# Performance work log

Hardware: AMD Instinct MI355X
Metric: run time of the kernel (lower is better)

Reference implementation:

```python
import jax, jax.numpy as jnp
import numpy as np

N = 100000       # nodes
F_IN = 512       # input features
H = 16           # hidden dim of conv1
C = 5            # num classes
E = 6400000      # edges (avg degree 64)


def setup_inputs() -> dict:
    key = jax.random.key(0)
    ks = jax.random.split(key, 8)
    x = jax.random.normal(ks[0], (N, F_IN), dtype=jnp.float32)
    edge_index = jax.random.randint(ks[1], (2, E), 0, N, dtype=jnp.int64)
    W1 = jax.random.normal(ks[2], (F_IN, H), dtype=jnp.float32) * (1.0 / np.sqrt(F_IN))
    b1 = jnp.zeros((H,), jnp.float32)
    W2 = jax.random.normal(ks[3], (H, C), dtype=jnp.float32) * (1.0 / np.sqrt(H))
    b2 = jnp.zeros((C,), jnp.float32)
    W3 = jax.random.normal(ks[4], (C, 32), dtype=jnp.float32) * (1.0 / np.sqrt(C))
    b3 = jnp.zeros((32,), jnp.float32)
    W4 = jax.random.normal(ks[5], (32, C), dtype=jnp.float32) * (1.0 / np.sqrt(32))
    b4 = jnp.zeros((C,), jnp.float32)
    return {"x": x, "edge_index": edge_index, "W1": W1, "b1": b1,
            "W2": W2, "b2": b2, "W3": W3, "b3": b3, "W4": W4, "b4": b4}


def _gcn_norm(edge_index):
    # add self-loops, unit edge weights (data has no edge_attr)
    loop = jnp.arange(N, dtype=edge_index.dtype)
    src = jnp.concatenate([edge_index[0], loop])
    dst = jnp.concatenate([edge_index[1], loop])
    deg = jax.ops.segment_sum(jnp.ones_like(dst, dtype=jnp.float32), dst,
                              num_segments=N)
    dinv = jnp.where(deg > 0, jax.lax.rsqrt(jnp.maximum(deg, 1.0)), 0.0)
    norm = dinv[src] * dinv[dst]  # [E+N]
    return src, dst, norm


def _gcn_conv(x, src, dst, norm, W, b):
    h = x @ W                               # transform first (small out dim)
    msg = h[src] * norm[:, None]            # gather + edge-normalize
    out = jax.ops.segment_sum(msg, dst, num_segments=N)  # scatter-add
    return out + b


def reference(x, edge_index, W1, b1, W2, b2, W3, b3, W4, b4):
    src, dst, norm = _gcn_norm(edge_index)
    h = _gcn_conv(x, src, dst, norm, W1, b1)
    h = jax.nn.relu(h)
    # F.dropout(training=self.training): identity in eval mode
    h = _gcn_conv(h, src, dst, norm, W2, b2)
    h = jax.nn.relu(h @ W3 + b3)
    h = h @ W4 + b4
    return jax.nn.log_softmax(h, axis=1)
```

## Files before the change

kernel.cpp:

```cpp
#include <hip/hip_runtime.h>
#include <hip/hip_bf16.h>


#define F_IN 512
#define HDIM 16
#define CDIM 5
#define NB   1024
#define SEG  8192
#define GWP_STRIDE 16
#define EPT  10
#define SCHUNK (1024*EPT)
#define CAP  8192

typedef __attribute__((ext_vector_type(8))) short short8;
typedef __attribute__((ext_vector_type(4))) float floatx4;

__device__ inline float bf2f(unsigned short u){
  unsigned int i = ((unsigned int)u) << 16; float f; __builtin_memcpy(&f, &i, 4); return f;
}
__device__ inline unsigned short f2bf(float x){
  unsigned int i; __builtin_memcpy(&i, &x, 4);
  unsigned int r = i + 0x7FFFu + ((i >> 16) & 1u);
  return (unsigned short)(r >> 16);
}
__device__ inline float ulo(unsigned int u){
  unsigned int v = u << 16; float f; __builtin_memcpy(&f, &v, 4); return f;
}
__device__ inline float uhi(unsigned int u){
  unsigned int v = u & 0xFFFF0000u; float f; __builtin_memcpy(&f, &v, 4); return f;
}
__device__ inline short8 pack8(float4 u0, float4 u1){
  unsigned short o[8] = {f2bf(u0.x), f2bf(u0.y), f2bf(u0.z), f2bf(u0.w),
                         f2bf(u1.x), f2bf(u1.y), f2bf(u1.z), f2bf(u1.w)};
  short8 r; __builtin_memcpy(&r, o, 16); return r;
}

__global__ __launch_bounds__(1024) void k_detect(const int* __restrict__ ei, int* __restrict__ flag,
                                                 int* __restrict__ gwp, int E){
  int t = threadIdx.x;
  if (t == 0) *flag = 0;
  gwp[t * GWP_STRIDE] = t * SEG;
  __syncthreads();
  long long step = E / 1024; if (step < 1) step = 1;
  long long pos = 2LL * ((long long)t * step) + 1;
  if (pos < 2LL * E){
    if (ei[pos] != 0) atomicOr(flag, 1);
  }
}

__global__ __launch_bounds__(256) void k_packW1(const float* __restrict__ W1,
                                                unsigned short* __restrict__ pw){
  int s = threadIdx.x;
  for (int slot = s; slot < 1024; slot += 256){
    int col = slot & 15, kg = (slot >> 4) & 3, t = slot >> 6;
    unsigned short o[8];
    #pragma unroll
    for (int e = 0; e < 8; ++e)
      o[e] = f2bf(W1[(t * 32 + kg * 8 + e) * HDIM + col]);
    uint4 v; __builtin_memcpy(&v, o, 16);
    *(uint4*)(pw + (size_t)slot * 8) = v;
  }
}

__global__ __launch_bounds__(1024) void k_binscatter(const int* __restrict__ ei, const int* __restrict__ flag,
                                                     int* __restrict__ gwp, int* __restrict__ pairs,
                                                     int E, int NPB){
  __shared__ int bh[NB];
  __shared__ int lex[NB + 1];
  __shared__ int bb2[NB];
  __shared__ int wsum[16];
  __shared__ unsigned short kb[SCHUNK];
  __shared__ int stage[SCHUNK];
  int t = threadIdx.x;
  int e0 = blockIdx.x * SCHUNK;
  int e1 = min(E, e0 + SCHUNK);
  int cnt = e1 - e0;
  if (cnt <= 0) return;
  int is32 = *flag;
  const uint2* ei2 = (const uint2*)ei;
  int pk[EPT]; int bi[EPT];
  #pragma unroll
  for (int j = 0; j < EPT; ++j){
    int e = e0 + t + j * 1024;
    if (e < e1){
      int src, dst;
      if (is32){ src = ei[e]; dst = ei[(size_t)E + e]; }
      else     { src = (int)ei2[e].x; dst = (int)ei2[(size_t)E + e].x; }
      int b = dst / NPB;
      pk[j] = src | ((dst - b * NPB) << 20);
      bi[j] = b;
    } else bi[j] = -1;
  }
  bh[t] = 0;
  __syncthreads();
  #pragma unroll
  for (int j = 0; j < EPT; ++j) if (bi[j] >= 0) atomicAdd(&bh[bi[j]], 1);
  __syncthreads();
  {
    int lane = t & 63, w = t >> 6;
    int v = bh[t];
    int xs = v;
    #pragma unroll
    for (int off = 1; off < 64; off <<= 1){
      int y = __shfl_up(xs, off);
      if (lane >= off) xs += y;
    }
    if (lane == 63) wsum[w] = xs;
    __syncthreads();
    int woff = 0;
    for (int k = 0; k < w; ++k) woff += wsum[k];
    int excl = woff + xs - v;
    lex[t] = excl;
    if (t == 1023) lex[NB] = woff + xs;
    bb2[t] = v ? atomicAdd(&gwp[t * GWP_STRIDE], v) : 0;
    __syncthreads();
    bh[t] = excl;
  }
  __syncthreads();
  #pragma unroll
  for (int j = 0; j < EPT; ++j){
    if (bi[j] >= 0){
      int idx = atomicAdd(&bh[bi[j]], 1);
      stage[idx] = pk[j];
      kb[idx] = (unsigned short)bi[j];
    }
  }
  __syncthreads();
  for (int k = t; k < cnt; k += 1024){
    int b = kb[k];
    pairs[bb2[b] + (k - lex[b])] = stage[k];
  }
}

__global__ __launch_bounds__(1024) void k_scanNB(const int* __restrict__ gwp, int* __restrict__ bbase,
                                                 int nb){
  __shared__ int wsum[16];
  int t = threadIdx.x, lane = t & 63, w = t >> 6;
  int v = (t < nb) ? (gwp[t * GWP_STRIDE] - t * SEG) : 0;
  int xs = v;
  #pragma unroll
  for (int off = 1; off < 64; off <<= 1){
    int y = __shfl_up(xs, off);
    if (lane >= off) xs += y;
  }
  if (lane == 63) wsum[w] = xs;
  __syncthreads();
  int woff = 0;
  for (int k = 0; k < w; ++k) woff += wsum[k];
  if (t < nb) bbase[t] = woff + xs - v;
  if (t == 1023) bbase[nb] = woff + xs;
}

__global__ __launch_bounds__(512) void k_bucket(const int* __restrict__ pairs, const int* __restrict__ bbase,
                                                int* __restrict__ rowptr, float* __restrict__ dinv,
                                                int* __restrict__ ssrc, int NPB, int n, int Etot){
  __shared__ int lcnt[4][128];
  __shared__ int tot[128];
  __shared__ int lexcl[128];
  __shared__ int w0sum;
  __shared__ int stage[CAP];
  int b = blockIdx.x;
  int t = threadIdx.x;
  int g = t >> 7;
  int node0 = b * NPB;
  int pbase = b * SEG;
  int obase = bbase[b];
  int cntE = bbase[b + 1] - obase;
  lcnt[g][t & 127] = 0;
  __syncthreads();
  for (int k = t; k < cntE; k += 512){
    unsigned int v = (unsigned int)pairs[pbase + k];
    atomicAdd(&lcnt[g][v >> 20], 1);
  }
  __syncthreads();
  if (t < 128){
    int s0 = lcnt[0][t], s1 = lcnt[1][t], s2 = lcnt[2][t], s3 = lcnt[3][t];
    tot[t] = s0 + s1 + s2 + s3;
    lcnt[0][t] = 0; lcnt[1][t] = s0; lcnt[2][t] = s0 + s1; lcnt[3][t] = s0 + s1 + s2;
  }
  __syncthreads();
  int lane = t & 63;
  int v = (t < 128) ? tot[t] : 0;
  int xs = v;
  #pragma unroll
  for (int off = 1; off < 64; off <<= 1){
    int y = __shfl_up(xs, off);
    if (lane >= off) xs += y;
  }
  if (t == 63) w0sum = xs;
  __syncthreads();
  if (t < 128) lexcl[t] = xs - v + ((t >= 64) ? w0sum : 0);
  __syncthreads();
  if (t < NPB){
    int node = node0 + t;
    if (node < n){
      rowptr[node] = obase + lexcl[t];
      dinv[node] = rsqrtf((float)(tot[t] + 1));
    }
  }
  lcnt[g][t & 127] += lexcl[t & 127];
  if (b == 0 && t == 0) rowptr[n] = Etot;
  __syncthreads();
  for (int k = t; k < cntE; k += 512){
    unsigned int v2 = (unsigned int)pairs[pbase + k];
    int idx = atomicAdd(&lcnt[g][v2 >> 20], 1);
    int src = (int)(v2 & 0xFFFFFu);
    if (idx < CAP) stage[idx] = src;
    else ssrc[obase + idx] = src;
  }
  __syncthreads();
  int m = cntE < CAP ? cntE : CAP;
  for (int k = t; k < m; k += 512) ssrc[obase + k] = stage[k];
}

__global__ __launch_bounds__(256) void k_gemm1(const float* __restrict__ x, const unsigned short* __restrict__ pw,
                                               const float* __restrict__ dinv, unsigned short* __restrict__ hs1,
                                               int n){
  int lane = threadIdx.x & 63;
  int col = lane & 15;
  int kg  = lane >> 4;
  int nt = (n + 15) >> 4;
  const short8* pw8 = (const short8*)pw;
  short8 B[16];
  #pragma unroll
  for (int t = 0; t < 16; ++t) B[t] = pw8[t * 64 + kg * 16 + col];
  int nw = gridDim.x * 4;
  for (int wid = blockIdx.x * 4 + (threadIdx.x >> 6); wid < nt; wid += nw){
    int row = wid * 16 + col;
    const float* xr = x + (size_t)min(row, n - 1) * F_IN;
    floatx4 acc = {0.f, 0.f, 0.f, 0.f};
    #pragma unroll
    for (int t = 0; t < 16; ++t){
      const float4* p = (const float4*)(xr + t * 32 + kg * 8);
      float4 u0 = p[0];
      float4 u1 = p[1];
      acc = __builtin_amdgcn_mfma_f32_16x16x32_bf16(pack8(u0, u1), B[t], acc, 0, 0, 0);
    }
    #pragma unroll
    for (int r = 0; r < 4; ++r){
      int orow = wid * 16 + kg * 4 + r;
      if (orow < n) hs1[(size_t)orow * HDIM + col] = f2bf(dinv[orow] * acc[r]);
    }
  }
}

__global__ __launch_bounds__(256) void k_agg1(const unsigned short* __restrict__ hs1,
    const int* __restrict__ rowptr, const int* __restrict__ ssrc,
    const float* __restrict__ dinv, const float* __restrict__ b1,
    const float* __restrict__ W2, unsigned short* __restrict__ hs2, int n){
  int lane = threadIdx.x & 63;
  int i = blockIdx.x * 4 + (threadIdx.x >> 6);
  if (i >= n) return;
  int slot = lane >> 1, half = lane & 1;
  int beg = rowptr[i], end = rowptr[i + 1];
  const uint4* hv = (const uint4*)hs1;
  float acc[8];
  #pragma unroll
  for (int k = 0; k < 8; ++k) acc[k] = 0.f;
  for (int e = beg + slot; e < end; e += 32){
    int src = ssrc[e];
    uint4 v = hv[(size_t)src * 2 + half];
    acc[0] += ulo(v.x); acc[1] += uhi(v.x);
    acc[2] += ulo(v.y); acc[3] += uhi(v.y);
    acc[4] += ulo(v.z); acc[5] += uhi(v.z);
    acc[6] += ulo(v.w); acc[7] += uhi(v.w);
  }
  #pragma unroll
  for (int off = 2; off < 64; off <<= 1){
    #pragma unroll
    for (int k = 0; k < 8; ++k) acc[k] += __shfl_xor(acc[k], off);
  }
  uint4 sv = hv[(size_t)i * 2 + half];
  float self[8] = {ulo(sv.x), uhi(sv.x), ulo(sv.y), uhi(sv.y),
                   ulo(sv.z), uhi(sv.z), ulo(sv.w), uhi(sv.w)};
  float dv = dinv[i];
  const float4* b1v = (const float4*)b1;
  float4 bl = b1v[half * 2], bh = b1v[half * 2 + 1];
  float r[8];
  r[0] = fmaxf(fmaf(dv, acc[0] + self[0], bl.x), 0.f);
  r[1] = fmaxf(fmaf(dv, acc[1] + self[1], bl.y), 0.f);
  r[2] = fmaxf(fmaf(dv, acc[2] + self[2], bl.z), 0.f);
  r[3] = fmaxf(fmaf(dv, acc[3] + self[3], bl.w), 0.f);
  r[4] = fmaxf(fmaf(dv, acc[4] + self[4], bh.x), 0.f);
  r[5] = fmaxf(fmaf(dv, acc[5] + self[5], bh.y), 0.f);
  r[6] = fmaxf(fmaf(dv, acc[6] + self[6], bh.z), 0.f);
  r[7] = fmaxf(fmaf(dv, acc[7] + self[7], bh.w), 0.f);
  const float* w2 = W2 + half * 8 * CDIM;
  float p[CDIM];
  #pragma unroll
  for (int c = 0; c < CDIM; ++c){
    float s = 0.f;
    #pragma unroll
    for (int k = 0; k < 8; ++k) s = fmaf(r[k], w2[k * CDIM + c], s);
    p[c] = s;
  }
  #pragma unroll
  for (int c = 0; c < CDIM; ++c) p[c] += __shfl_xor(p[c], 1);
  if (lane == 0){
    unsigned short o[8];
    #pragma unroll
    for (int c = 0; c < CDIM; ++c) o[c] = f2bf(dv * p[c]);
    o[5] = 0; o[6] = 0; o[7] = 0;
    uint4 v; __builtin_memcpy(&v, o, 16);
    *(uint4*)(hs2 + (size_t)i * 8) = v;
  }
}

__global__ __launch_bounds__(256) void k_agg2(const unsigned short* __restrict__ hs2,
    const int* __restrict__ rowptr, const int* __restrict__ ssrc,
    const float* __restrict__ dinv, const float* __restrict__ b2,
    const float* __restrict__ W3, const float* __restrict__ b3,
    const float* __restrict__ W4, const float* __restrict__ b4,
    float* __restrict__ out, int n){
  int lane = threadIdx.x & 63;
  int i = blockIdx.x * 4 + (threadIdx.x >> 6);
  if (i >= n) return;
  int beg = rowptr[i], end = rowptr[i + 1];
  const uint4* hv = (const uint4*)hs2;
  float acc[CDIM];
  #pragma unroll
  for (int k = 0; k < CDIM; ++k) acc[k] = 0.f;
  for (int e = beg + lane; e < end; e += 64){
    int src = ssrc[e];
    uint4 v = hv[src];
    acc[0] += ulo(v.x); acc[1] += uhi(v.x);
    acc[2] += ulo(v.y); acc[3] += uhi(v.y);
    acc[4] += ulo(v.z);
  }
  #pragma unroll
  for (int off = 1; off < 64; off <<= 1){
    #pragma unroll
    for (int k = 0; k < CDIM; ++k) acc[k] += __shfl_xor(acc[k], off);
  }
  float dv = dinv[i];
  uint4 sv = hv[i];
  float a0 = fmaf(dv, acc[0] + ulo(sv.x), b2[0]);
  float a1 = fmaf(dv, acc[1] + uhi(sv.x), b2[1]);
  float a2 = fmaf(dv, acc[2] + ulo(sv.y), b2[2]);
  float a3 = fmaf(dv, acc[3] + uhi(sv.y), b2[3]);
  float a4 = fmaf(dv, acc[4] + ulo(sv.z), b2[4]);
  int m = lane & 31;
  float h3 = b3[m];
  h3 = fmaf(a0, W3[0 * 32 + m], h3);
  h3 = fmaf(a1, W3[1 * 32 + m], h3);
  h3 = fmaf(a2, W3[2 * 32 + m], h3);
  h3 = fmaf(a3, W3[3 * 32 + m], h3);
  h3 = fmaf(a4, W3[4 * 32 + m], h3);
  h3 = fmaxf(h3, 0.f);
  float q0 = h3 * W4[m * CDIM + 0], q1 = h3 * W4[m * CDIM + 1], q2 = h3 * W4[m * CDIM + 2];
  float q3 = h3 * W4[m * CDIM + 3], q4 = h3 * W4[m * CDIM + 4];
  #pragma unroll
  for (int off = 1; off < 32; off <<= 1){
    q0 += __shfl_xor(q0, off); q1 += __shfl_xor(q1, off); q2 += __shfl_xor(q2, off);
    q3 += __shfl_xor(q3, off); q4 += __shfl_xor(q4, off);
  }
  q0 += b4[0]; q1 += b4[1]; q2 += b4[2]; q3 += b4[3]; q4 += b4[4];
  float mx = fmaxf(fmaxf(fmaxf(q0, q1), fmaxf(q2, q3)), q4);
  float sum = expf(q0 - mx) + expf(q1 - mx) + expf(q2 - mx) + expf(q3 - mx) + expf(q4 - mx);
  float lse = mx + logf(sum);
  if (lane < CDIM){
    float v = q0;
    if (lane == 1) v = q1;
    if (lane == 2) v = q2;
    if (lane == 3) v = q3;
    if (lane == 4) v = q4;
    out[(size_t)i * CDIM + lane] = v - lse;
  }
}

extern "C" void kernel_launch(void* const* d_in, const int* in_sizes, int n_in,
                              void* d_out, int out_size, void* d_ws, size_t ws_size,
                              hipStream_t stream){
  const float* x  = (const float*)d_in[0];
  const int*   ei = (const int*)d_in[1];
  const float* W1 = (const float*)d_in[2];
  const float* b1 = (const float*)d_in[3];
  const float* W2 = (const float*)d_in[4];
  const float* b2 = (const float*)d_in[5];
  const float* W3 = (const float*)d_in[6];
  const float* b3 = (const float*)d_in[7];
  const float* W4 = (const float*)d_in[8];
  const float* b4 = (const float*)d_in[9];
  float* out = (float*)d_out;

  int N = in_sizes[0] / F_IN;
  int E = in_sizes[1] / 2;
  int NPB = (N + NB - 1) / NB;

  char* ws = (char*)d_ws;
  size_t off = 0;
  auto alloc = [&](size_t bytes) -> char* {
    char* p = ws + off;
    off += (bytes + 255) & ~(size_t)255;
    return p;
  };
  int* flag  = (int*)alloc(4);
  int* gwp   = (int*)alloc((size_t)NB * GWP_STRIDE * 4);
  int* bbase = (int*)alloc(((size_t)NB + 1) * 4);
  int* rowptr= (int*)alloc(((size_t)N + 1) * 4);
  float* dinv= (float*)alloc((size_t)N * 4);
  unsigned short* pw = (unsigned short*)alloc((size_t)F_IN * HDIM * 2);
  int* pairs = (int*)alloc((size_t)NB * SEG * 4);
  int* ssrc  = (int*)alloc((size_t)E * 4);
  unsigned short* hs1 = (unsigned short*)alloc((size_t)N * HDIM * 2);
  unsigned short* hs2 = (unsigned short*)alloc((size_t)N * 8 * 2);
  (void)ws_size; (void)n_in; (void)out_size;

  k_detect<<<1, 1024, 0, stream>>>(ei, flag, gwp, E);
  k_packW1<<<1, 256, 0, stream>>>(W1, pw);
  int sblocks = (E + SCHUNK - 1) / SCHUNK;
  k_binscatter<<<sblocks, 1024, 0, stream>>>(ei, flag, gwp, pairs, E, NPB);
  k_scanNB<<<1, 1024, 0, stream>>>(gwp, bbase, NB);
  k_bucket<<<NB, 512, 0, stream>>>(pairs, bbase, rowptr, dinv, ssrc, NPB, N, E);
  k_gemm1<<<768, 256, 0, stream>>>(x, pw, dinv, hs1, N);
  k_agg1<<<(N + 3) / 4, 256, 0, stream>>>(hs1, rowptr, ssrc, dinv, b1, W2, hs2, N);
  k_agg2<<<(N + 3) / 4, 256, 0, stream>>>(hs2, rowptr, ssrc, dinv, b2, W3, b3, W4, b4, out, N);
}
```

Before: 265.4 us.

## Drop CSR build; aggregate directly from destination buckets with shared-memory atomics

Removes the scan and per-node bucket sort that built rowptr and sorted sources. Aggregation now reads the coarse destination-binned pairs per bucket (512 buckets of about 196 nodes) and accumulates messages into LDS with float atomics. A small kernel computes degrees from the same bins. This saves a full pass that rewrites 6.4M edges, at the cost of heavy LDS atomic contention and fewer, larger blocks. The final per-node MLP is also moved into a single thread per node.

```diff
diff --git a/kernel.cpp b/kernel.cpp
--- a/kernel.cpp
+++ b/kernel.cpp
@@ -5,12 +5,12 @@
 #define F_IN 512
 #define HDIM 16
 #define CDIM 5
-#define NB   1024
-#define SEG  8192
+#define NB   512
+#define NPB_MAX 200
+#define SEG  16384
 #define GWP_STRIDE 16
 #define EPT  10
 #define SCHUNK (1024*EPT)
-#define CAP  8192
 
 typedef __attribute__((ext_vector_type(8))) short short8;
 typedef __attribute__((ext_vector_type(4))) float floatx4;
@@ -39,7 +39,7 @@
                                                  int* __restrict__ gwp, int E){
   int t = threadIdx.x;
   if (t == 0) *flag = 0;
-  gwp[t * GWP_STRIDE] = t * SEG;
+  if (t < NB) gwp[t * GWP_STRIDE] = t * SEG;
   __syncthreads();
   long long step = E / 1024; if (step < 1) step = 1;
   long long pos = 2LL * ((long long)t * step) + 1;
@@ -91,14 +91,14 @@
       bi[j] = b;
     } else bi[j] = -1;
   }
-  bh[t] = 0;
+  if (t < NB) bh[t] = 0;
   __syncthreads();
   #pragma unroll
   for (int j = 0; j < EPT; ++j) if (bi[j] >= 0) atomicAdd(&bh[bi[j]], 1);
   __syncthreads();
   {
     int lane = t & 63, w = t >> 6;
-    int v = bh[t];
+    int v = (t < NB) ? bh[t] : 0;
     int xs = v;
     #pragma unroll
     for (int off = 1; off < 64; off <<= 1){
@@ -110,11 +110,12 @@
     int woff = 0;
     for (int k = 0; k < w; ++k) woff += wsum[k];
     int excl = woff + xs - v;
-    lex[t] = excl;
-    if (t == 1023) lex[NB] = woff + xs;
-    bb2[t] = v ? atomicAdd(&gwp[t * GWP_STRIDE], v) : 0;
-    __syncthreads();
-    bh[t] = excl;
+    if (t < NB){
+      lex[t] = excl;
+      bb2[t] = v ? atomicAdd(&gwp[t * GWP_STRIDE], v) : 0;
+      bh[t] = excl;
+    }
+    if (t == NB - 1) lex[NB] = excl + v;
   }
   __syncthreads();
   #pragma unroll
@@ -132,85 +133,20 @@
   }
 }
 
-__global__ __launch_bounds__(1024) void k_scanNB(const int* __restrict__ gwp, int* __restrict__ bbase,
-                                                 int nb){
-  __shared__ int wsum[16];
-  int t = threadIdx.x, lane = t & 63, w = t >> 6;
-  int v = (t < nb) ? (gwp[t * GWP_STRIDE] - t * SEG) : 0;
-  int xs = v;
-  #pragma unroll
-  for (int off = 1; off < 64; off <<= 1){
-    int y = __shfl_up(xs, off);
-    if (lane >= off) xs += y;
-  }
-  if (lane == 63) wsum[w] = xs;
-  __syncthreads();
-  int woff = 0;
-  for (int k = 0; k < w; ++k) woff += wsum[k];
-  if (t < nb) bbase[t] = woff + xs - v;
-  if (t == 1023) bbase[nb] = woff + xs;
-}
-
-__global__ __launch_bounds__(512) void k_bucket(const int* __restrict__ pairs, const int* __restrict__ bbase,
-                                                int* __restrict__ rowptr, float* __restrict__ dinv,
-                                                int* __restrict__ ssrc, int NPB, int n, int Etot){
-  __shared__ int lcnt[4][128];
-  __shared__ int tot[128];
-  __shared__ int lexcl[128];
-  __shared__ int w0sum;
-  __shared__ int stage[CAP];
-  int b = blockIdx.x;
-  int t = threadIdx.x;
-  int g = t >> 7;
-  int node0 = b * NPB;
-  int pbase = b * SEG;
-  int obase = bbase[b];
-  int cntE = bbase[b + 1] - obase;
-  lcnt[g][t & 127] = 0;
-  __syncthreads();
-  for (int k = t; k < cntE; k += 512){
-    unsigned int v = (unsigned int)pairs[pbase + k];
-    atomicAdd(&lcnt[g][v >> 20], 1);
-  }
-  __syncthreads();
-  if (t < 128){
-    int s0 = lcnt[0][t], s1 = lcnt[1][t], s2 = lcnt[2][t], s3 = lcnt[3][t];
-    tot[t] = s0 + s1 + s2 + s3;
-    lcnt[0][t] = 0; lcnt[1][t] = s0; lcnt[2][t] = s0 + s1; lcnt[3][t] = s0 + s1 + s2;
-  }
-  __syncthreads();
-  int lane = t & 63;
-  int v = (t < 128) ? tot[t] : 0;
-  int xs = v;
-  #pragma unroll
-  for (int off = 1; off < 64; off <<= 1){
-    int y = __shfl_up(xs, off);
-    if (lane >= off) xs += y;
-  }
-  if (t == 63) w0sum = xs;
-  __syncthreads();
-  if (t < 128) lexcl[t] = xs - v + ((t >= 64) ? w0sum : 0);
-  __syncthreads();
-  if (t < NPB){
-    int node = node0 + t;
-    if (node < n){
-      rowptr[node] = obase + lexcl[t];
-      dinv[node] = rsqrtf((float)(tot[t] + 1));
-    }
-  }
-  lcnt[g][t & 127] += lexcl[t & 127];
-  if (b == 0 && t == 0) rowptr[n] = Etot;
-  __syncthreads();
-  for (int k = t; k < cntE; k += 512){
-    unsigned int v2 = (unsigned int)pairs[pbase + k];
-    int idx = atomicAdd(&lcnt[g][v2 >> 20], 1);
-    int src = (int)(v2 & 0xFFFFFu);
-    if (idx < CAP) stage[idx] = src;
-    else ssrc[obase + idx] = src;
-  }
-  __syncthreads();
-  int m = cntE < CAP ? cntE : CAP;
-  for (int k = t; k < m; k += 512) ssrc[obase + k] = stage[k];
+__global__ __launch_bounds__(256) void k_deg(const int* __restrict__ pairs, const int* __restrict__ gwp,
+                                             float* __restrict__ dinv, int n, int NPB){
+  __shared__ int h[NPB_MAX];
+  int b = blockIdx.x, t = threadIdx.x;
+  int cntE = gwp[b * GWP_STRIDE] - b * SEG;
+  for (int k = t; k < NPB; k += 256) h[k] = 0;
+  __syncthreads();
+  const int* pb = pairs + (size_t)b * SEG;
+  for (int k = t; k < cntE; k += 256) atomicAdd(&h[((unsigned)pb[k]) >> 20], 1);
+  __syncthreads();
+  for (int k = t; k < NPB; k += 256){
+    int node = b * NPB + k;
+    if (node < n) dinv[node] = rsqrtf((float)(h[k] + 1));
+  }
 }
 
 __global__ __launch_bounds__(256) void k_gemm1(const float* __restrict__ x, const unsigned short* __restrict__ pw,
@@ -244,127 +180,113 @@
   }
 }
 
-__global__ __launch_bounds__(256) void k_agg1(const unsigned short* __restrict__ hs1,
-    const int* __restrict__ rowptr, const int* __restrict__ ssrc,
+__global__ __launch_bounds__(512) void k_agg1f(const unsigned short* __restrict__ hs1,
+    const int* __restrict__ pairs, const int* __restrict__ gwp,
     const float* __restrict__ dinv, const float* __restrict__ b1,
-    const float* __restrict__ W2, unsigned short* __restrict__ hs2, int n){
-  int lane = threadIdx.x & 63;
-  int i = blockIdx.x * 4 + (threadIdx.x >> 6);
-  if (i >= n) return;
-  int slot = lane >> 1, half = lane & 1;
-  int beg = rowptr[i], end = rowptr[i + 1];
+    const float* __restrict__ W2, unsigned short* __restrict__ hs2, int n, int NPB){
+  __shared__ float acc[NPB_MAX * 17];
+  int b = blockIdx.x, t = threadIdx.x;
+  int cntE = gwp[b * GWP_STRIDE] - b * SEG;
+  for (int k = t; k < NPB * 17; k += 512) acc[k] = 0.f;
+  __syncthreads();
   const uint4* hv = (const uint4*)hs1;
-  float acc[8];
-  #pragma unroll
-  for (int k = 0; k < 8; ++k) acc[k] = 0.f;
-  for (int e = beg + slot; e < end; e += 32){
-    int src = ssrc[e];
+  const int* pb = pairs + (size_t)b * SEG;
+  int half = t & 1;
+  for (int k = (t >> 1); k < cntE; k += 256){
+    int p = pb[k];
+    int src = p & 0xFFFFF;
+    int dl = ((unsigned)p) >> 20;
     uint4 v = hv[(size_t)src * 2 + half];
-    acc[0] += ulo(v.x); acc[1] += uhi(v.x);
-    acc[2] += ulo(v.y); acc[3] += uhi(v.y);
-    acc[4] += ulo(v.z); acc[5] += uhi(v.z);
-    acc[6] += ulo(v.w); acc[7] += uhi(v.w);
-  }
-  #pragma unroll
-  for (int off = 2; off < 64; off <<= 1){
-    #pragma unroll
-    for (int k = 0; k < 8; ++k) acc[k] += __shfl_xor(acc[k], off);
-  }
-  uint4 sv = hv[(size_t)i * 2 + half];
-  float self[8] = {ulo(sv.x), uhi(sv.x), ulo(sv.y), uhi(sv.y),
-                   ulo(sv.z), uhi(sv.z), ulo(sv.w), uhi(sv.w)};
-  float dv = dinv[i];
-  const float4* b1v = (const float4*)b1;
-  float4 bl = b1v[half * 2], bh = b1v[half * 2 + 1];
-  float r[8];
-  r[0] = fmaxf(fmaf(dv, acc[0] + self[0], bl.x), 0.f);
-  r[1] = fmaxf(fmaf(dv, acc[1] + self[1], bl.y), 0.f);
-  r[2] = fmaxf(fmaf(dv, acc[2] + self[2], bl.z), 0.f);
-  r[3] = fmaxf(fmaf(dv, acc[3] + self[3], bl.w), 0.f);
-  r[4] = fmaxf(fmaf(dv, acc[4] + self[4], bh.x), 0.f);
-  r[5] = fmaxf(fmaf(dv, acc[5] + self[5], bh.y), 0.f);
-  r[6] = fmaxf(fmaf(dv, acc[6] + self[6], bh.z), 0.f);
-  r[7] = fmaxf(fmaf(dv, acc[7] + self[7], bh.w), 0.f);
-  const float* w2 = W2 + half * 8 * CDIM;
-  float p[CDIM];
-  #pragma unroll
-  for (int c = 0; c < CDIM; ++c){
-    float s = 0.f;
-    #pragma unroll
-    for (int k = 0; k < 8; ++k) s = fmaf(r[k], w2[k * CDIM + c], s);
-    p[c] = s;
-  }
-  #pragma unroll
-  for (int c = 0; c < CDIM; ++c) p[c] += __shfl_xor(p[c], 1);
-  if (lane == 0){
+    float* a = acc + dl * 17 + half * 8;
+    atomicAdd(a + 0, ulo(v.x)); atomicAdd(a + 1, uhi(v.x));
+    atomicAdd(a + 2, ulo(v.y)); atomicAdd(a + 3, uhi(v.y));
+    atomicAdd(a + 4, ulo(v.z)); atomicAdd(a + 5, uhi(v.z));
+    atomicAdd(a + 6, ulo(v.w)); atomicAdd(a + 7, uhi(v.w));
+  }
+  __syncthreads();
+  for (int i = t; i < NPB; i += 512){
+    int node = b * NPB + i;
+    if (node >= n) break;
+    float dv = dinv[node];
+    uint4 s0 = hv[(size_t)node * 2], s1 = hv[(size_t)node * 2 + 1];
+    float self[16] = {ulo(s0.x), uhi(s0.x), ulo(s0.y), uhi(s0.y),
+                      ulo(s0.z), uhi(s0.z), ulo(s0.w), uhi(s0.w),
+                      ulo(s1.x), uhi(s1.x), ulo(s1.y), uhi(s1.y),
+                      ulo(s1.z), uhi(s1.z), ulo(s1.w), uhi(s1.w)};
+    float r[16];
+    #pragma unroll
+    for (int j = 0; j < 16; ++j)
+      r[j] = fmaxf(fmaf(dv, acc[i * 17 + j] + self[j], b1[j]), 0.f);
     unsigned short o[8];
     #pragma unroll
-    for (int c = 0; c < CDIM; ++c) o[c] = f2bf(dv * p[c]);
+    for (int c = 0; c < CDIM; ++c){
+      float s = 0.f;
+      #pragma unroll
+      for (int j = 0; j < 16; ++j) s = fmaf(r[j], W2[j * CDIM + c], s);
+      o[c] = f2bf(dv * s);
+    }
     o[5] = 0; o[6] = 0; o[7] = 0;
     uint4 v; __builtin_memcpy(&v, o, 16);
-    *(uint4*)(hs2 + (size_t)i * 8) = v;
-  }
-}
-
-__global__ __launch_bounds__(256) void k_agg2(const unsigned short* __restrict__ hs2,
-    const int* __restrict__ rowptr, const int* __restrict__ ssrc,
+    *(uint4*)(hs2 + (size_t)node * 8) = v;
+  }
+}
+
+__global__ __launch_bounds__(512) void k_agg2f(const unsigned short* __restrict__ hs2,
+    const int* __restrict__ pairs, const int* __restrict__ gwp,
     const float* __restrict__ dinv, const float* __restrict__ b2,
     const float* __restrict__ W3, const float* __restrict__ b3,
     const float* __restrict__ W4, const float* __restrict__ b4,
-    float* __restrict__ out, int n){
-  int lane = threadIdx.x & 63;
-  int i = blockIdx.x * 4 + (threadIdx.x >> 6);
-  if (i >= n) return;
-  int beg = rowptr[i], end = rowptr[i + 1];
+    float* __restrict__ out, int n, int NPB){
+  __shared__ float acc[NPB_MAX * 9];
+  int b = blockIdx.x, t = threadIdx.x;
+  int cntE = gwp[b * GWP_STRIDE] - b * SEG;
+  for (int k = t; k < NPB * 9; k += 512) acc[k] = 0.f;
+  __syncthreads();
   const uint4* hv = (const uint4*)hs2;
-  float acc[CDIM];
-  #pragma unroll
-  for (int k = 0; k < CDIM; ++k) acc[k] = 0.f;
-  for (int e = beg + lane; e < end; e += 64){
-    int src = ssrc[e];
+  const int* pb = pairs + (size_t)b * SEG;
+  for (int k = t; k < cntE; k += 512){
+    int p = pb[k];
+    int src = p & 0xFFFFF;
+    int dl = ((unsigned)p) >> 20;
     uint4 v = hv[src];
-    acc[0] += ulo(v.x); acc[1] += uhi(v.x);
-    acc[2] += ulo(v.y); acc[3] += uhi(v.y);
-    acc[4] += ulo(v.z);
-  }
-  #pragma unroll
-  for (int off = 1; off < 64; off <<= 1){
-    #pragma unroll
-    for (int k = 0; k < CDIM; ++k) acc[k] += __shfl_xor(acc[k], off);
-  }
-  float dv = dinv[i];
-  uint4 sv = hv[i];
-  float a0 = fmaf(dv, acc[0] + ulo(sv.x), b2[0]);
-  float a1 = fmaf(dv, acc[1] + uhi(sv.x), b2[1]);
-  float a2 = fmaf(dv, acc[2] + ulo(sv.y), b2[2]);
-  float a3 = fmaf(dv, acc[3] + uhi(sv.y), b2[3]);
-  float a4 = fmaf(dv, acc[4] + ulo(sv.z), b2[4]);
-  int m = lane & 31;
-  float h3 = b3[m];
-  h3 = fmaf(a0, W3[0 * 32 + m], h3);
-  h3 = fmaf(a1, W3[1 * 32 + m], h3);
-  h3 = fmaf(a2, W3[2 * 32 + m], h3);
-  h3 = fmaf(a3, W3[3 * 32 + m], h3);
-  h3 = fmaf(a4, W3[4 * 32 + m], h3);
-  h3 = fmaxf(h3, 0.f);
-  float q0 = h3 * W4[m * CDIM + 0], q1 = h3 * W4[m * CDIM + 1], q2 = h3 * W4[m * CDIM + 2];
-  float q3 = h3 * W4[m * CDIM + 3], q4 = h3 * W4[m * CDIM + 4];
-  #pragma unroll
-  for (int off = 1; off < 32; off <<= 1){
-    q0 += __shfl_xor(q0, off); q1 += __shfl_xor(q1, off); q2 += __shfl_xor(q2, off);
-    q3 += __shfl_xor(q3, off); q4 += __shfl_xor(q4, off);
-  }
-  q0 += b4[0]; q1 += b4[1]; q2 += b4[2]; q3 += b4[3]; q4 += b4[4];
-  float mx = fmaxf(fmaxf(fmaxf(q0, q1), fmaxf(q2, q3)), q4);
-  float sum = expf(q0 - mx) + expf(q1 - mx) + expf(q2 - mx) + expf(q3 - mx) + expf(q4 - mx);
-  float lse = mx + logf(sum);
-  if (lane < CDIM){
-    float v = q0;
-    if (lane == 1) v = q1;
-    if (lane == 2) v = q2;
-    if (lane == 3) v = q3;
-    if (lane == 4) v = q4;
-    out[(size_t)i * CDIM + lane] = v - lse;
+    float* a = acc + dl * 9;
+    atomicAdd(a + 0, ulo(v.x)); atomicAdd(a + 1, uhi(v.x));
+    atomicAdd(a + 2, ulo(v.y)); atomicAdd(a + 3, uhi(v.y));
+    atomicAdd(a + 4, ulo(v.z));
+  }
+  __syncthreads();
+  for (int i = t; i < NPB; i += 512){
+    int node = b * NPB + i;
+    if (node >= n) break;
+    float dv = dinv[node];
+    uint4 sv = hv[node];
+    float a0 = fmaf(dv, acc[i * 9 + 0] + ulo(sv.x), b2[0]);
+    float a1 = fmaf(dv, acc[i * 9 + 1] + uhi(sv.x), b2[1]);
+    float a2 = fmaf(dv, acc[i * 9 + 2] + ulo(sv.y), b2[2]);
+    float a3 = fmaf(dv, acc[i * 9 + 3] + uhi(sv.y), b2[3]);
+    float a4 = fmaf(dv, acc[i * 9 + 4] + ulo(sv.z), b2[4]);
+    float q[CDIM];
+    #pragma unroll
+    for (int c = 0; c < CDIM; ++c) q[c] = b4[c];
+    #pragma unroll
+    for (int m = 0; m < 32; ++m){
+      float h3 = b3[m];
+      h3 = fmaf(a0, W3[0 * 32 + m], h3);
+      h3 = fmaf(a1, W3[1 * 32 + m], h3);
+      h3 = fmaf(a2, W3[2 * 32 + m], h3);
+      h3 = fmaf(a3, W3[3 * 32 + m], h3);
+      h3 = fmaf(a4, W3[4 * 32 + m], h3);
+      h3 = fmaxf(h3, 0.f);
+      #pragma unroll
+      for (int c = 0; c < CDIM; ++c) q[c] = fmaf(h3, W4[m * CDIM + c], q[c]);
+    }
+    float mx = fmaxf(fmaxf(fmaxf(q[0], q[1]), fmaxf(q[2], q[3])), q[4]);
+    float sum = expf(q[0] - mx) + expf(q[1] - mx) + expf(q[2] - mx) +
+                expf(q[3] - mx) + expf(q[4] - mx);
+    float lse = mx + logf(sum);
+    float* op = out + (size_t)node * CDIM;
+    #pragma unroll
+    for (int c = 0; c < CDIM; ++c) op[c] = q[c] - lse;
   }
 }
 
@@ -396,12 +318,9 @@
   };
   int* flag  = (int*)alloc(4);
   int* gwp   = (int*)alloc((size_t)NB * GWP_STRIDE * 4);
-  int* bbase = (int*)alloc(((size_t)NB + 1) * 4);
-  int* rowptr= (int*)alloc(((size_t)N + 1) * 4);
   float* dinv= (float*)alloc((size_t)N * 4);
   unsigned short* pw = (unsigned short*)alloc((size_t)F_IN * HDIM * 2);
   int* pairs = (int*)alloc((size_t)NB * SEG * 4);
-  int* ssrc  = (int*)alloc((size_t)E * 4);
   unsigned short* hs1 = (unsigned short*)alloc((size_t)N * HDIM * 2);
   unsigned short* hs2 = (unsigned short*)alloc((size_t)N * 8 * 2);
   (void)ws_size; (void)n_in; (void)out_size;
@@ -410,9 +329,8 @@
   k_packW1<<<1, 256, 0, stream>>>(W1, pw);
   int sblocks = (E + SCHUNK - 1) / SCHUNK;
   k_binscatter<<<sblocks, 1024, 0, stream>>>(ei, flag, gwp, pairs, E, NPB);
-  k_scanNB<<<1, 1024, 0, stream>>>(gwp, bbase, NB);
-  k_bucket<<<NB, 512, 0, stream>>>(pairs, bbase, rowptr, dinv, ssrc, NPB, N, E);
+  k_deg<<<NB, 256, 0, stream>>>(pairs, gwp, dinv, N, NPB);
   k_gemm1<<<768, 256, 0, stream>>>(x, pw, dinv, hs1, N);
-  k_agg1<<<(N + 3) / 4, 256, 0, stream>>>(hs1, rowptr, ssrc, dinv, b1, W2, hs2, N);
-  k_agg2<<<(N + 3) / 4, 256, 0, stream>>>(hs2, rowptr, ssrc, dinv, b2, W3, b3, W4, b4, out, N);
-}
+  k_agg1f<<<NB, 512, 0, stream>>>(hs1, pairs, gwp, dinv, b1, W2, hs2, N, NPB);
+  k_agg2f<<<NB, 512, 0, stream>>>(hs2, pairs, gwp, dinv, b2, W3, b3, W4, b4, out, N, NPB);
+}
```

After: 802.2 us. 3.02x slower.

## Drop global bucket scan and pack kernel; use padded per-bucket CSR with row degrees

Applied to the files above, without the earlier changes.

Removes the k_scanNB and k_packW1 launches. W1 packing is folded into k_detect, and the CSR is laid out with a fixed SEG-sized segment per bucket, so each row is described by a start offset plus a stored degree instead of a globally compacted row pointer. k_bucket now uses 8 per-wave histogram copies instead of 4, which should reduce LDS atomic contention. The cost is a larger ssrc buffer and an extra rowdeg read in the aggregation kernels, and gather locality may drop slightly because segments are padded.

```diff
diff --git a/kernel.cpp b/kernel.cpp
--- a/kernel.cpp
+++ b/kernel.cpp
@@ -36,10 +36,20 @@
 }
 
 __global__ __launch_bounds__(1024) void k_detect(const int* __restrict__ ei, int* __restrict__ flag,
-                                                 int* __restrict__ gwp, int E){
+                                                 int* __restrict__ gwp, const float* __restrict__ W1,
+                                                 unsigned short* __restrict__ pw, int E){
   int t = threadIdx.x;
   if (t == 0) *flag = 0;
   gwp[t * GWP_STRIDE] = t * SEG;
+  {
+    int col = t & 15, kg = (t >> 4) & 3, tt = t >> 6;
+    unsigned short o[8];
+    #pragma unroll
+    for (int e = 0; e < 8; ++e)
+      o[e] = f2bf(W1[(tt * 32 + kg * 8 + e) * HDIM + col]);
+    uint4 v; __builtin_memcpy(&v, o, 16);
+    *(uint4*)(pw + (size_t)t * 8) = v;
+  }
   __syncthreads();
   long long step = E / 1024; if (step < 1) step = 1;
   long long pos = 2LL * ((long long)t * step) + 1;
@@ -48,25 +58,11 @@
   }
 }
 
-__global__ __launch_bounds__(256) void k_packW1(const float* __restrict__ W1,
-                                                unsigned short* __restrict__ pw){
-  int s = threadIdx.x;
-  for (int slot = s; slot < 1024; slot += 256){
-    int col = slot & 15, kg = (slot >> 4) & 3, t = slot >> 6;
-    unsigned short o[8];
-    #pragma unroll
-    for (int e = 0; e < 8; ++e)
-      o[e] = f2bf(W1[(t * 32 + kg * 8 + e) * HDIM + col]);
-    uint4 v; __builtin_memcpy(&v, o, 16);
-    *(uint4*)(pw + (size_t)slot * 8) = v;
-  }
-}
-
 __global__ __launch_bounds__(1024) void k_binscatter(const int* __restrict__ ei, const int* __restrict__ flag,
                                                      int* __restrict__ gwp, int* __restrict__ pairs,
                                                      int E, int NPB){
   __shared__ int bh[NB];
-  __shared__ int lex[NB + 1];
+  __shared__ int lex[NB];
   __shared__ int bb2[NB];
   __shared__ int wsum[16];
   __shared__ unsigned short kb[SCHUNK];
@@ -111,7 +107,6 @@
     for (int k = 0; k < w; ++k) woff += wsum[k];
     int excl = woff + xs - v;
     lex[t] = excl;
-    if (t == 1023) lex[NB] = woff + xs;
     bb2[t] = v ? atomicAdd(&gwp[t * GWP_STRIDE], v) : 0;
     __syncthreads();
     bh[t] = excl;
@@ -132,41 +127,23 @@
   }
 }
 
-__global__ __launch_bounds__(1024) void k_scanNB(const int* __restrict__ gwp, int* __restrict__ bbase,
-                                                 int nb){
-  __shared__ int wsum[16];
-  int t = threadIdx.x, lane = t & 63, w = t >> 6;
-  int v = (t < nb) ? (gwp[t * GWP_STRIDE] - t * SEG) : 0;
-  int xs = v;
-  #pragma unroll
-  for (int off = 1; off < 64; off <<= 1){
-    int y = __shfl_up(xs, off);
-    if (lane >= off) xs += y;
-  }
-  if (lane == 63) wsum[w] = xs;
-  __syncthreads();
-  int woff = 0;
-  for (int k = 0; k < w; ++k) woff += wsum[k];
-  if (t < nb) bbase[t] = woff + xs - v;
-  if (t == 1023) bbase[nb] = woff + xs;
-}
-
-__global__ __launch_bounds__(512) void k_bucket(const int* __restrict__ pairs, const int* __restrict__ bbase,
-                                                int* __restrict__ rowptr, float* __restrict__ dinv,
-                                                int* __restrict__ ssrc, int NPB, int n, int Etot){
-  __shared__ int lcnt[4][128];
+__global__ __launch_bounds__(512) void k_bucket(const int* __restrict__ pairs, const int* __restrict__ gwp,
+                                                int* __restrict__ rowptr, int* __restrict__ rowdeg,
+                                                float* __restrict__ dinv, int* __restrict__ ssrc,
+                                                int NPB, int n){
+  __shared__ int lcnt[8][128];
   __shared__ int tot[128];
   __shared__ int lexcl[128];
   __shared__ int w0sum;
   __shared__ int stage[CAP];
   int b = blockIdx.x;
   int t = threadIdx.x;
-  int g = t >> 7;
+  int g = t >> 6;
   int node0 = b * NPB;
   int pbase = b * SEG;
-  int obase = bbase[b];
-  int cntE = bbase[b + 1] - obase;
-  lcnt[g][t & 127] = 0;
+  int obase = b * SEG;
+  int cntE = gwp[b * GWP_STRIDE] - b * SEG;
+  for (int k = t & 63; k < 128; k += 64) lcnt[g][k] = 0;
   __syncthreads();
   for (int k = t; k < cntE; k += 512){
     unsigned int v = (unsigned int)pairs[pbase + k];
@@ -174,9 +151,14 @@
   }
   __syncthreads();
   if (t < 128){
-    int s0 = lcnt[0][t], s1 = lcnt[1][t], s2 = lcnt[2][t], s3 = lcnt[3][t];
-    tot[t] = s0 + s1 + s2 + s3;
-    lcnt[0][t] = 0; lcnt[1][t] = s0; lcnt[2][t] = s0 + s1; lcnt[3][t] = s0 + s1 + s2;
+    int c = 0;
+    #pragma unroll
+    for (int gg = 0; gg < 8; ++gg){
+      int tmp = lcnt[gg][t];
+      lcnt[gg][t] = c;
+      c += tmp;
+    }
+    tot[t] = c;
   }
   __syncthreads();
   int lane = t & 63;
@@ -195,11 +177,14 @@
     int node = node0 + t;
     if (node < n){
       rowptr[node] = obase + lexcl[t];
+      rowdeg[node] = tot[t];
       dinv[node] = rsqrtf((float)(tot[t] + 1));
     }
   }
-  lcnt[g][t & 127] += lexcl[t & 127];
-  if (b == 0 && t == 0) rowptr[n] = Etot;
+  if (t < 128){
+    #pragma unroll
+    for (int gg = 0; gg < 8; ++gg) lcnt[gg][t] += lexcl[t];
+  }
   __syncthreads();
   for (int k = t; k < cntE; k += 512){
     unsigned int v2 = (unsigned int)pairs[pbase + k];
@@ -245,14 +230,14 @@
 }
 
 __global__ __launch_bounds__(256) void k_agg1(const unsigned short* __restrict__ hs1,
-    const int* __restrict__ rowptr, const int* __restrict__ ssrc,
+    const int* __restrict__ rowptr, const int* __restrict__ rowdeg, const int* __restrict__ ssrc,
     const float* __restrict__ dinv, const float* __restrict__ b1,
     const float* __restrict__ W2, unsigned short* __restrict__ hs2, int n){
   int lane = threadIdx.x & 63;
   int i = blockIdx.x * 4 + (threadIdx.x >> 6);
   if (i >= n) return;
   int slot = lane >> 1, half = lane & 1;
-  int beg = rowptr[i], end = rowptr[i + 1];
+  int beg = rowptr[i], end = beg + rowdeg[i];
   const uint4* hv = (const uint4*)hs1;
   float acc[8];
   #pragma unroll
@@ -307,7 +292,7 @@
 }
 
 __global__ __launch_bounds__(256) void k_agg2(const unsigned short* __restrict__ hs2,
-    const int* __restrict__ rowptr, const int* __restrict__ ssrc,
+    const int* __restrict__ rowptr, const int* __restrict__ rowdeg, const int* __restrict__ ssrc,
     const float* __restrict__ dinv, const float* __restrict__ b2,
     const float* __restrict__ W3, const float* __restrict__ b3,
     const float* __restrict__ W4, const float* __restrict__ b4,
@@ -315,7 +300,7 @@
   int lane = threadIdx.x & 63;
   int i = blockIdx.x * 4 + (threadIdx.x >> 6);
   if (i >= n) return;
-  int beg = rowptr[i], end = rowptr[i + 1];
+  int beg = rowptr[i], end = beg + rowdeg[i];
   const uint4* hv = (const uint4*)hs2;
   float acc[CDIM];
   #pragma unroll
@@ -396,23 +381,21 @@
   };
   int* flag  = (int*)alloc(4);
   int* gwp   = (int*)alloc((size_t)NB * GWP_STRIDE * 4);
-  int* bbase = (int*)alloc(((size_t)NB + 1) * 4);
-  int* rowptr= (int*)alloc(((size_t)N + 1) * 4);
+  int* rowptr= (int*)alloc((size_t)N * 4);
+  int* rowdeg= (int*)alloc((size_t)N * 4);
   float* dinv= (float*)alloc((size_t)N * 4);
   unsigned short* pw = (unsigned short*)alloc((size_t)F_IN * HDIM * 2);
   int* pairs = (int*)alloc((size_t)NB * SEG * 4);
-  int* ssrc  = (int*)alloc((size_t)E * 4);
+  int* ssrc  = (int*)alloc((size_t)NB * SEG * 4);
   unsigned short* hs1 = (unsigned short*)alloc((size_t)N * HDIM * 2);
   unsigned short* hs2 = (unsigned short*)alloc((size_t)N * 8 * 2);
   (void)ws_size; (void)n_in; (void)out_size;
 
-  k_detect<<<1, 1024, 0, stream>>>(ei, flag, gwp, E);
-  k_packW1<<<1, 256, 0, stream>>>(W1, pw);
+  k_detect<<<1, 1024, 0, stream>>>(ei, flag, gwp, W1, pw, E);
   int sblocks = (E + SCHUNK - 1) / SCHUNK;
   k_binscatter<<<sblocks, 1024, 0, stream>>>(ei, flag, gwp, pairs, E, NPB);
-  k_scanNB<<<1, 1024, 0, stream>>>(gwp, bbase, NB);
-  k_bucket<<<NB, 512, 0, stream>>>(pairs, bbase, rowptr, dinv, ssrc, NPB, N, E);
+  k_bucket<<<NB, 512, 0, stream>>>(pairs, gwp, rowptr, rowdeg, dinv, ssrc, NPB, N);
   k_gemm1<<<768, 256, 0, stream>>>(x, pw, dinv, hs1, N);
-  k_agg1<<<(N + 3) / 4, 256, 0, stream>>>(hs1, rowptr, ssrc, dinv, b1, W2, hs2, N);
-  k_agg2<<<(N + 3) / 4, 256, 0, stream>>>(hs2, rowptr, ssrc, dinv, b2, W3, b3, W4, b4, out, N);
-}
+  k_agg1<<<(N + 3) / 4, 256, 0, stream>>>(hs1, rowptr, rowdeg, ssrc, dinv, b1, W2, hs2, N);
+  k_agg2<<<(N + 3) / 4, 256, 0, stream>>>(hs2, rowptr, rowdeg, ssrc, dinv, b2, W3, b3, W4, b4, out, N);
+}
```

After: 257.9 us. 2.8% less time.
